# Performance work log

Hardware: AMD Instinct MI355X
Metric: run time of the kernel (lower is better)

The kernel has to match this reference:

```python
import jax, jax.numpy as jnp
import numpy as np

DIM = 4096
ROOT = 64  # int(sqrt(DIM))
B = 8192
LN_EPS = 1e-5


def setup_inputs() -> dict:
    key = jax.random.key(0)
    ks = jax.random.split(key, 7)
    return {
        "x": jax.random.normal(ks[0], (B, DIM), dtype=jnp.float32),
        "param_1": jax.random.normal(ks[1], (ROOT, 4 * ROOT, ROOT), dtype=jnp.float32),
        "bias_1": jax.random.normal(ks[2], (ROOT, 4 * ROOT), dtype=jnp.float32),
        "param_2": jax.random.normal(ks[3], (ROOT, ROOT, 4 * ROOT), dtype=jnp.float32),
        "bias_2": jax.random.normal(ks[4], (ROOT, ROOT), dtype=jnp.float32),
        "ln_gamma": jnp.ones((DIM,), dtype=jnp.float32),
        "ln_beta": jnp.zeros((DIM,), dtype=jnp.float32),
        "W": jax.random.normal(ks[5], (DIM, DIM), dtype=jnp.float32) * (1.0 / np.sqrt(DIM)),
        "b": jax.random.normal(ks[6], (DIM,), dtype=jnp.float32),
    }


def reference(x, param_1, bias_1, param_2, bias_2, ln_gamma, ln_beta, W, b):
    r = x
    # block-diagonal per-row matmuls: x -> [B, root, root]
    xb = x.reshape(-1, ROOT, ROOT)
    # fc_row: param_1[r] @ row + bias_1[r]  -> [B, root, 4*root]
    h = jnp.einsum("brk,rmk->brm", xb, param_1) + bias_1
    h = jax.nn.relu(h)
    # second per-row projection -> [B, root, root]
    h = jnp.einsum("brm,rkm->brk", h, param_2) + bias_2
    h = jax.nn.relu(h)
    h = h.reshape(-1, DIM)
    # LayerNorm (affine, eps=1e-5)
    mu = jnp.mean(h, axis=-1, keepdims=True)
    var = jnp.mean(jnp.square(h - mu), axis=-1, keepdims=True)
    h = (h - mu) * jax.lax.rsqrt(var + LN_EPS) * ln_gamma + ln_beta
    # Linear + ReLU + residual
    h = jax.nn.relu(h @ W.T + b)
    return h + r
```

## Files before the change

### kernel.cpp

```cpp
#include <hip/hip_runtime.h>

typedef __bf16 bf16;
typedef bf16 bf16x4 __attribute__((ext_vector_type(4)));
typedef bf16 bf16x8 __attribute__((ext_vector_type(8)));
typedef float floatx4 __attribute__((ext_vector_type(4)));

#define MFMA(a, b, c) __builtin_amdgcn_mfma_f32_16x16x32_bf16((a), (b), (c), 0, 0, 0)

__device__ __forceinline__ void gl2lds16(const void* g, void* l) {
  __builtin_amdgcn_global_load_lds(
      (const __attribute__((address_space(1))) void*)g,
      (__attribute__((address_space(3))) void*)l, 16, 0, 0);
}

__device__ __forceinline__ bf16x4 cvt4(const float4 v) {
  bf16x4 o;
  o[0] = (bf16)v.x; o[1] = (bf16)v.y; o[2] = (bf16)v.z; o[3] = (bf16)v.w;
  return o;
}

__global__ __launch_bounds__(256) void cast_w_kernel(const float* __restrict__ W,
                                                     bf16* __restrict__ Wb, int n4) {
  int idx = blockIdx.x * 256 + threadIdx.x;
  int stride = gridDim.x * 256;
  const float4* W4 = (const float4*)W;
  for (int i = idx; i < n4; i += stride) {
    *(bf16x4*)(Wb + (size_t)i * 4) = cvt4(W4[i]);
  }
}

__global__ __launch_bounds__(256) void blockdiag_kernel(
    const float* __restrict__ x, const float* __restrict__ p1,
    const float* __restrict__ b1, const float* __restrict__ p2,
    const float* __restrict__ b2, bf16* __restrict__ h2) {
  __shared__ bf16 sX[128 * 72];
  __shared__ bf16 sP1[64 * 72];
  __shared__ bf16 sP2[64 * 72];
  __shared__ bf16 sH1[128 * 72];
  __shared__ float sB1[256];
  __shared__ float sB2[64];

  const int tid = threadIdx.x;
  const int bt = blockIdx.x, r = blockIdx.y;
  const size_t b0 = (size_t)bt * 128;

  const float* xr = x + b0 * 4096 + r * 64;
#pragma unroll
  for (int i = 0; i < 8; ++i) {
    int idx = tid + i * 256;
    int row = idx >> 4, c4 = idx & 15;
    float4 v = *(const float4*)(xr + (size_t)row * 4096 + c4 * 4);
    *(bf16x4*)(&sX[row * 72 + c4 * 4]) = cvt4(v);
  }
  sB1[tid] = b1[r * 256 + tid];
  if (tid < 64) sB2[tid] = b2[r * 64 + tid];

  const float* p1r = p1 + (size_t)r * 16384;
  const float* p2r = p2 + (size_t)r * 16384;

  const int w = tid >> 6, lane = tid & 63;
  const int q = lane >> 4, l16 = lane & 15;
  const int wm = w >> 1, wn = w & 1;

  const floatx4 fzero = {0.f, 0.f, 0.f, 0.f};
  floatx4 acc2[4][2];
#pragma unroll
  for (int mt = 0; mt < 4; ++mt)
#pragma unroll
    for (int nt = 0; nt < 2; ++nt) acc2[mt][nt] = fzero;

  for (int qh = 0; qh < 4; ++qh) {
    __syncthreads();
#pragma unroll
    for (int i = 0; i < 4; ++i) {
      int idx = tid + i * 256;
      int row = idx >> 4, c4 = idx & 15;
      float4 v = *(const float4*)(p1r + (size_t)(qh * 64 + row) * 64 + c4 * 4);
      *(bf16x4*)(&sP1[row * 72 + c4 * 4]) = cvt4(v);
      float4 u = *(const float4*)(p2r + (size_t)row * 256 + qh * 64 + c4 * 4);
      *(bf16x4*)(&sP2[row * 72 + c4 * 4]) = cvt4(u);
    }
    __syncthreads();

    floatx4 acc1[4][2];
#pragma unroll
    for (int mt = 0; mt < 4; ++mt)
#pragma unroll
      for (int nt = 0; nt < 2; ++nt) acc1[mt][nt] = fzero;
#pragma unroll
    for (int ks = 0; ks < 2; ++ks) {
      bf16x8 a[4], bb[2];
#pragma unroll
      for (int mt = 0; mt < 4; ++mt)
        a[mt] = *(const bf16x8*)(&sX[(64 * wm + mt * 16 + l16) * 72 + ks * 32 + q * 8]);
#pragma unroll
      for (int nt = 0; nt < 2; ++nt)
        bb[nt] = *(const bf16x8*)(&sP1[(32 * wn + nt * 16 + l16) * 72 + ks * 32 + q * 8]);
#pragma unroll
      for (int mt = 0; mt < 4; ++mt)
#pragma unroll
        for (int nt = 0; nt < 2; ++nt) acc1[mt][nt] = MFMA(a[mt], bb[nt], acc1[mt][nt]);
    }
#pragma unroll
    for (int mt = 0; mt < 4; ++mt) {
#pragma unroll
      for (int nt = 0; nt < 2; ++nt) {
        int c = 32 * wn + nt * 16 + l16;
        float bias1v = sB1[qh * 64 + c];
#pragma unroll
        for (int v = 0; v < 4; ++v) {
          int row = 64 * wm + mt * 16 + q * 4 + v;
          sH1[row * 72 + c] = (bf16)fmaxf(acc1[mt][nt][v] + bias1v, 0.f);
        }
      }
    }
    __syncthreads();
#pragma unroll
    for (int ks = 0; ks < 2; ++ks) {
      bf16x8 a2[4], bb2[2];
#pragma unroll
      for (int mt = 0; mt < 4; ++mt)
        a2[mt] = *(const bf16x8*)(&sH1[(64 * wm + mt * 16 + l16) * 72 + ks * 32 + q * 8]);
#pragma unroll
      for (int nt = 0; nt < 2; ++nt)
        bb2[nt] = *(const bf16x8*)(&sP2[(32 * wn + nt * 16 + l16) * 72 + ks * 32 + q * 8]);
#pragma unroll
      for (int mt = 0; mt < 4; ++mt)
#pragma unroll
        for (int nt = 0; nt < 2; ++nt) acc2[mt][nt] = MFMA(a2[mt], bb2[nt], acc2[mt][nt]);
    }
  }

  bf16* ho = h2 + b0 * 4096 + r * 64;
#pragma unroll
  for (int mt = 0; mt < 4; ++mt) {
#pragma unroll
    for (int nt = 0; nt < 2; ++nt) {
      int kk = 32 * wn + nt * 16 + l16;
      float b2v = sB2[kk];
#pragma unroll
      for (int v = 0; v < 4; ++v) {
        int row = 64 * wm + mt * 16 + q * 4 + v;
        ho[(size_t)row * 4096 + kk] = (bf16)fmaxf(acc2[mt][nt][v] + b2v, 0.f);
      }
    }
  }
}

__global__ __launch_bounds__(256) void ln_kernel(bf16* __restrict__ h,
                                                 const float* __restrict__ gamma,
                                                 const float* __restrict__ beta) {
  const int row = blockIdx.x;
  const int tid = threadIdx.x;
  bf16* hr = h + (size_t)row * 4096;
  float vals[16];
  float s = 0.f, ss = 0.f;
#pragma unroll
  for (int i = 0; i < 2; ++i) {
    bf16x8 v = *(const bf16x8*)(hr + (size_t)(i * 256 + tid) * 8);
#pragma unroll
    for (int j = 0; j < 8; ++j) {
      float f = (float)v[j];
      vals[i * 8 + j] = f;
      s += f;
      ss += f * f;
    }
  }
#pragma unroll
  for (int off = 32; off > 0; off >>= 1) {
    s += __shfl_down(s, off, 64);
    ss += __shfl_down(ss, off, 64);
  }
  __shared__ float red[8];
  const int w = tid >> 6, lane = tid & 63;
  if (lane == 0) { red[w] = s; red[4 + w] = ss; }
  __syncthreads();
  s = red[0] + red[1] + red[2] + red[3];
  ss = red[4] + red[5] + red[6] + red[7];
  const float mu = s * (1.f / 4096.f);
  const float var = ss * (1.f / 4096.f) - mu * mu;
  const float rsig = rsqrtf(var + 1e-5f);
#pragma unroll
  for (int i = 0; i < 2; ++i) {
    const int base = (i * 256 + tid) * 8;
    float4 g0 = *(const float4*)(gamma + base);
    float4 g1 = *(const float4*)(gamma + base + 4);
    float4 be0 = *(const float4*)(beta + base);
    float4 be1 = *(const float4*)(beta + base + 4);
    float g[8] = {g0.x, g0.y, g0.z, g0.w, g1.x, g1.y, g1.z, g1.w};
    float bb[8] = {be0.x, be0.y, be0.z, be0.w, be1.x, be1.y, be1.z, be1.w};
    bf16x8 o;
#pragma unroll
    for (int j = 0; j < 8; ++j) o[j] = (bf16)((vals[i * 8 + j] - mu) * rsig * g[j] + bb[j]);
    *(bf16x8*)(hr + base) = o;
  }
}

__global__ __launch_bounds__(256) void gemm_kernel(
    const bf16* __restrict__ A,
    const bf16* __restrict__ B,
    const float* __restrict__ bias, const float* __restrict__ xres,
    float* __restrict__ out) {
  __shared__ bf16 sA[128 * 32];
  __shared__ bf16 sB[128 * 32];
  const int tid = threadIdx.x;
  const int n0 = blockIdx.x * 128;
  const int m0 = blockIdx.y * 128;
  const int w = tid >> 6, lane = tid & 63;
  const int q = lane >> 4, l16 = lane & 15;
  const int wm = w >> 1, wn = w & 1;

  const floatx4 fzero = {0.f, 0.f, 0.f, 0.f};
  floatx4 acc[4][4];
#pragma unroll
  for (int mt = 0; mt < 4; ++mt)
#pragma unroll
    for (int nt = 0; nt < 4; ++nt) acc[mt][nt] = fzero;

  const int ra = tid >> 2;
  const int koff = (tid & 3) * 8;
  const bf16* aptr = A + (size_t)(m0 + ra) * 4096 + koff;
  const bf16* bptr = B + (size_t)(n0 + ra) * 4096 + koff;
  bf16* la = sA + tid * 8;
  bf16* lb = sB + tid * 8;

  for (int k0 = 0; k0 < 4096; k0 += 32) {
    gl2lds16(aptr, la);
    gl2lds16(aptr + (size_t)64 * 4096, sA + 2048 + tid * 8);
    gl2lds16(bptr, lb);
    gl2lds16(bptr + (size_t)64 * 4096, sB + 2048 + tid * 8);
    aptr += 32;
    bptr += 32;
    __syncthreads();
    bf16x8 af[4], bfr[4];
#pragma unroll
    for (int mt = 0; mt < 4; ++mt)
      af[mt] = *(const bf16x8*)(&sA[(64 * wm + mt * 16 + l16) * 32 + q * 8]);
#pragma unroll
    for (int nt = 0; nt < 4; ++nt)
      bfr[nt] = *(const bf16x8*)(&sB[(64 * wn + nt * 16 + l16) * 32 + q * 8]);
#pragma unroll
    for (int mt = 0; mt < 4; ++mt)
#pragma unroll
      for (int nt = 0; nt < 4; ++nt) acc[mt][nt] = MFMA(af[mt], bfr[nt], acc[mt][nt]);
    __syncthreads();
  }

#pragma unroll
  for (int nt = 0; nt < 4; ++nt) {
    const int col = n0 + 64 * wn + nt * 16 + l16;
    const float bv = bias[col];
#pragma unroll
    for (int mt = 0; mt < 4; ++mt) {
#pragma unroll
      for (int v = 0; v < 4; ++v) {
        const int row = m0 + 64 * wm + mt * 16 + q * 4 + v;
        const size_t o = (size_t)row * 4096 + col;
        out[o] = fmaxf(acc[mt][nt][v] + bv, 0.f) + xres[o];
      }
    }
  }
}

extern "C" void kernel_launch(void* const* d_in, const int* in_sizes, int n_in,
                              void* d_out, int out_size, void* d_ws, size_t ws_size,
                              hipStream_t stream) {
  const float* x = (const float*)d_in[0];
  const float* p1 = (const float*)d_in[1];
  const float* b1 = (const float*)d_in[2];
  const float* p2 = (const float*)d_in[3];
  const float* b2 = (const float*)d_in[4];
  const float* gamma = (const float*)d_in[5];
  const float* beta = (const float*)d_in[6];
  const float* W = (const float*)d_in[7];
  const float* bias = (const float*)d_in[8];
  float* out = (float*)d_out;

  const size_t WB_BYTES = (size_t)4096 * 4096 * 2;
  const size_t H_BYTES = (size_t)8192 * 4096 * 2;
  bf16* Wb = (bf16*)d_ws;
  bf16* h = (bf16*)((char*)d_ws + WB_BYTES);

  size_t avail = ws_size > WB_BYTES ? ws_size - WB_BYTES : 0;
  int nch = 1;
  while (nch < 64 && H_BYTES / (size_t)nch > avail) nch <<= 1;
  const int rows = 8192 / nch;

  cast_w_kernel<<<2048, 256, 0, stream>>>(W, Wb, 4096 * 4096 / 4);
  for (int c = 0; c < nch; ++c) {
    const float* xc = x + (size_t)c * rows * 4096;
    float* outc = out + (size_t)c * rows * 4096;
    blockdiag_kernel<<<dim3(rows / 128, 64), 256, 0, stream>>>(xc, p1, b1, p2, b2, h);
    ln_kernel<<<rows, 256, 0, stream>>>(h, gamma, beta);
    gemm_kernel<<<dim3(32, rows / 128), 256, 0, stream>>>(h, Wb, bias, xc, outc);
  }
}
```

Before: 746.8 us.

## Double-buffer block-diagonal weights and remap GEMM workgroups across XCDs

The block-diagonal kernel now double-buffers the param_1 and param_2 slices in shared memory. It prefetches the next quarter into registers while the current quarter's MFMAs run, and issues the x and first weight loads together before converting them. This is meant to hide global load latency and removes one barrier per iteration, at the cost of more LDS and registers. Separately, the GEMM remaps block IDs so that consecutive tiles land on the same XCD, aiming for better L2 reuse on MI355X's 8-XCD layout.

```diff
diff --git a/kernel.cpp b/kernel.cpp
--- a/kernel.cpp
+++ b/kernel.cpp
@@ -34,9 +34,9 @@
     const float* __restrict__ b1, const float* __restrict__ p2,
     const float* __restrict__ b2, bf16* __restrict__ h2) {
   __shared__ bf16 sX[128 * 72];
-  __shared__ bf16 sP1[64 * 72];
-  __shared__ bf16 sP2[64 * 72];
   __shared__ bf16 sH1[128 * 72];
+  __shared__ bf16 sP1[2][64 * 72];
+  __shared__ bf16 sP2[2][64 * 72];
   __shared__ float sB1[256];
   __shared__ float sB2[64];
 
@@ -45,18 +45,39 @@
   const size_t b0 = (size_t)bt * 128;
 
   const float* xr = x + b0 * 4096 + r * 64;
+  const float* p1r = p1 + (size_t)r * 16384;
+  const float* p2r = p2 + (size_t)r * 16384;
+
+  float4 xv[8];
 #pragma unroll
   for (int i = 0; i < 8; ++i) {
     int idx = tid + i * 256;
     int row = idx >> 4, c4 = idx & 15;
-    float4 v = *(const float4*)(xr + (size_t)row * 4096 + c4 * 4);
-    *(bf16x4*)(&sX[row * 72 + c4 * 4]) = cvt4(v);
+    xv[i] = *(const float4*)(xr + (size_t)row * 4096 + c4 * 4);
+  }
+  float4 pv[4], uv[4];
+#pragma unroll
+  for (int i = 0; i < 4; ++i) {
+    int idx = tid + i * 256;
+    int row = idx >> 4, c4 = idx & 15;
+    pv[i] = *(const float4*)(p1r + (size_t)row * 64 + c4 * 4);
+    uv[i] = *(const float4*)(p2r + (size_t)row * 256 + c4 * 4);
   }
   sB1[tid] = b1[r * 256 + tid];
   if (tid < 64) sB2[tid] = b2[r * 64 + tid];
-
-  const float* p1r = p1 + (size_t)r * 16384;
-  const float* p2r = p2 + (size_t)r * 16384;
+#pragma unroll
+  for (int i = 0; i < 8; ++i) {
+    int idx = tid + i * 256;
+    int row = idx >> 4, c4 = idx & 15;
+    *(bf16x4*)(&sX[row * 72 + c4 * 4]) = cvt4(xv[i]);
+  }
+#pragma unroll
+  for (int i = 0; i < 4; ++i) {
+    int idx = tid + i * 256;
+    int row = idx >> 4, c4 = idx & 15;
+    *(bf16x4*)(&sP1[0][row * 72 + c4 * 4]) = cvt4(pv[i]);
+    *(bf16x4*)(&sP2[0][row * 72 + c4 * 4]) = cvt4(uv[i]);
+  }
 
   const int w = tid >> 6, lane = tid & 63;
   const int q = lane >> 4, l16 = lane & 15;
@@ -69,18 +90,19 @@
 #pragma unroll
     for (int nt = 0; nt < 2; ++nt) acc2[mt][nt] = fzero;
 
+  __syncthreads();
+
   for (int qh = 0; qh < 4; ++qh) {
-    __syncthreads();
-#pragma unroll
-    for (int i = 0; i < 4; ++i) {
-      int idx = tid + i * 256;
-      int row = idx >> 4, c4 = idx & 15;
-      float4 v = *(const float4*)(p1r + (size_t)(qh * 64 + row) * 64 + c4 * 4);
-      *(bf16x4*)(&sP1[row * 72 + c4 * 4]) = cvt4(v);
-      float4 u = *(const float4*)(p2r + (size_t)row * 256 + qh * 64 + c4 * 4);
-      *(bf16x4*)(&sP2[row * 72 + c4 * 4]) = cvt4(u);
-    }
-    __syncthreads();
+    const int cur = qh & 1;
+    if (qh < 3) {
+#pragma unroll
+      for (int i = 0; i < 4; ++i) {
+        int idx = tid + i * 256;
+        int row = idx >> 4, c4 = idx & 15;
+        pv[i] = *(const float4*)(p1r + (size_t)((qh + 1) * 64 + row) * 64 + c4 * 4);
+        uv[i] = *(const float4*)(p2r + (size_t)row * 256 + (qh + 1) * 64 + c4 * 4);
+      }
+    }
 
     floatx4 acc1[4][2];
 #pragma unroll
@@ -95,7 +117,7 @@
         a[mt] = *(const bf16x8*)(&sX[(64 * wm + mt * 16 + l16) * 72 + ks * 32 + q * 8]);
 #pragma unroll
       for (int nt = 0; nt < 2; ++nt)
-        bb[nt] = *(const bf16x8*)(&sP1[(32 * wn + nt * 16 + l16) * 72 + ks * 32 + q * 8]);
+        bb[nt] = *(const bf16x8*)(&sP1[cur][(32 * wn + nt * 16 + l16) * 72 + ks * 32 + q * 8]);
 #pragma unroll
       for (int mt = 0; mt < 4; ++mt)
 #pragma unroll
@@ -115,6 +137,7 @@
       }
     }
     __syncthreads();
+
 #pragma unroll
     for (int ks = 0; ks < 2; ++ks) {
       bf16x8 a2[4], bb2[2];
@@ -123,12 +146,23 @@
         a2[mt] = *(const bf16x8*)(&sH1[(64 * wm + mt * 16 + l16) * 72 + ks * 32 + q * 8]);
 #pragma unroll
       for (int nt = 0; nt < 2; ++nt)
-        bb2[nt] = *(const bf16x8*)(&sP2[(32 * wn + nt * 16 + l16) * 72 + ks * 32 + q * 8]);
+        bb2[nt] = *(const bf16x8*)(&sP2[cur][(32 * wn + nt * 16 + l16) * 72 + ks * 32 + q * 8]);
 #pragma unroll
       for (int mt = 0; mt < 4; ++mt)
 #pragma unroll
         for (int nt = 0; nt < 2; ++nt) acc2[mt][nt] = MFMA(a2[mt], bb2[nt], acc2[mt][nt]);
     }
+
+    if (qh < 3) {
+#pragma unroll
+      for (int i = 0; i < 4; ++i) {
+        int idx = tid + i * 256;
+        int row = idx >> 4, c4 = idx & 15;
+        *(bf16x4*)(&sP1[cur ^ 1][row * 72 + c4 * 4]) = cvt4(pv[i]);
+        *(bf16x4*)(&sP2[cur ^ 1][row * 72 + c4 * 4]) = cvt4(uv[i]);
+      }
+    }
+    __syncthreads();
   }
 
   bf16* ho = h2 + b0 * 4096 + r * 64;
@@ -204,8 +238,14 @@
   __shared__ bf16 sA[128 * 32];
   __shared__ bf16 sB[128 * 32];
   const int tid = threadIdx.x;
-  const int n0 = blockIdx.x * 128;
-  const int m0 = blockIdx.y * 128;
+
+  const int nwg = gridDim.x * gridDim.y;
+  const int orig = blockIdx.y * gridDim.x + blockIdx.x;
+  const int cpx = nwg >> 3;
+  const int nid = (orig & 7) * cpx + (orig >> 3);
+  const int n0 = (nid % gridDim.x) * 128;
+  const int m0 = (nid / gridDim.x) * 128;
+
   const int w = tid >> 6, lane = tid & 63;
   const int q = lane >> 4, l16 = lane & 15;
   const int wm = w >> 1, wn = w & 1;
```

Result: no change. 747.6 us (+0.1%).
